# Performance work log

Hardware: AMD Instinct MI355X
Metric: run time of the kernel (lower is better)

Reference implementation:

```python
import jax, jax.numpy as jnp
import numpy as np

# SMPL kinematic tree parents (fixed, 24 joints)
PARENTS = (-1, 0, 0, 0, 1, 2, 3, 4, 5, 6, 7, 8, 9, 9, 9, 12, 13, 14, 16, 17, 18, 19, 20, 21)
RES = 64
B, N = 2, 32768


def _trilinear(grid, pts):
    """Faithful F.grid_sample (5D, bilinear, align_corners=False, zero padding).
    grid: [C, R, R, R]; pts: [M, 3] normalized coords in [-1, 1].
    After the permutes in correspondence_to_smpl_function, coordinate k of a
    point indexes spatial axis k of the stored grid. Returns [M, C]."""
    C, R = grid.shape[0], grid.shape[1]
    gt = grid.reshape(C, -1).T  # [R^3, C]
    coords = ((pts + 1.0) * R - 1.0) * 0.5  # align_corners=False unnormalize
    f0 = jnp.floor(coords)
    w1 = coords - f0
    w0 = 1.0 - w1
    i0 = f0.astype(jnp.int32)
    out = jnp.zeros((pts.shape[0], C), dtype=grid.dtype)
    for dx in (0, 1):
        for dy in (0, 1):
            for dz in (0, 1):
                ix, iy, iz = i0[:, 0] + dx, i0[:, 1] + dy, i0[:, 2] + dz
                valid = ((ix >= 0) & (ix < R) & (iy >= 0) & (iy < R)
                         & (iz >= 0) & (iz < R))
                w = ((w1[:, 0] if dx else w0[:, 0])
                     * (w1[:, 1] if dy else w0[:, 1])
                     * (w1[:, 2] if dz else w0[:, 2]))
                idx = (jnp.clip(ix, 0, R - 1) * R + jnp.clip(iy, 0, R - 1)) * R \
                      + jnp.clip(iz, 0, R - 1)
                out = out + gt[idx] * (w * valid.astype(w.dtype))[:, None]
    return out


def _rodrigues(r):
    """Axis-angle [J,3] -> rotation matrices [J,3,3] (matches th_posemap_axisang)."""
    theta = jnp.sqrt(jnp.sum(r * r, axis=-1) + 1e-12)  # [J]
    ax = r / theta[:, None]
    x, y, z = ax[:, 0], ax[:, 1], ax[:, 2]
    zero = jnp.zeros_like(x)
    K = jnp.stack([zero, -z, y, z, zero, -x, -y, x, zero], axis=-1).reshape(-1, 3, 3)
    s = jnp.sin(theta)[:, None, None]
    c = jnp.cos(theta)[:, None, None]
    I = jnp.eye(3, dtype=r.dtype)
    return I + s * K + (1.0 - c) * jnp.matmul(K, K)


def _skeleton(beta, rotmats, v_template, smpl_shapedirs, J_regressor):
    """compute_smpl_skeleton: returns relative joint transforms [B, 24, 4, 4]."""
    b = beta.shape[0]
    v = v_template[None] + jnp.einsum('vdk,bk->bvd', smpl_shapedirs, beta)  # [B,6890,3]
    j = jnp.einsum('jv,bvd->bjd', J_regressor, v)  # [B,24,3]
    bottom = jnp.tile(jnp.array([[[0., 0., 0., 1.]]], dtype=beta.dtype), (b, 1, 1))

    def mk(R, t):  # th_with_zeros
        return jnp.concatenate([jnp.concatenate([R, t[..., None]], -1), bottom], 1)

    results = [mk(rotmats[:, 0], j[:, 0])]
    for i in range(1, 24):  # fixed 24-joint chain
        p = PARENTS[i]
        rel = mk(rotmats[:, i], j[:, i] - j[:, p])
        results.append(jnp.matmul(results[p], rel))
    A = jnp.stack(results, axis=1)  # [B,24,4,4]
    # subtract th_pack(A @ [j;0]): only last column changes
    t = jnp.einsum('bjrc,bjc->bjr', A[..., :3], j)  # [B,24,4]
    return jnp.concatenate([A[..., :3], (A[..., 3] - t)[..., None]], -1)


def setup_inputs() -> dict:
    key = jax.random.key(0)
    ks = jax.random.split(key, 12)
    return {
        'points': jax.random.uniform(ks[0], (B, N, 3), jnp.float32, -0.9, 0.9),
        'pose': jax.random.normal(ks[1], (B, 72), jnp.float32) * 0.2,
        'beta': jax.random.normal(ks[2], (B, 10), jnp.float32),
        'trans': jax.random.normal(ks[3], (B, 3), jnp.float32) * 0.1,
        'scale': jnp.float32(1.0),
        'center': jnp.zeros((3,), jnp.float32),
        'closest_grid': jax.random.normal(ks[4], (3, RES, RES, RES), jnp.float32) * 0.5,
        'shapedirs_grid': jax.random.normal(ks[5], (30, RES, RES, RES), jnp.float32) * 0.01,
        'posedirs_grid': jax.random.normal(ks[6], (621, RES, RES, RES), jnp.float32) * 0.01,
        'skin_grid': jax.random.uniform(ks[7], (24, RES, RES, RES), jnp.float32),
        'v_template': jax.random.normal(ks[8], (6890, 3), jnp.float32) * 0.3,
        'smpl_shapedirs': jax.random.normal(ks[9], (6890, 3, 10), jnp.float32) * 0.01,
        'J_regressor': (lambda u: u / jnp.sum(u, 1, keepdims=True))(
            jax.random.uniform(ks[10], (24, 6890), jnp.float32)),
    }


def reference(points, pose, beta, trans, scale, center, closest_grid,
              shapedirs_grid, posedirs_grid, skin_grid, v_template,
              smpl_shapedirs, J_regressor):
    b, n = points.shape[0], points.shape[1]
    pts = (points * scale + center).reshape(-1, 3)  # [M,3]

    closest = _trilinear(closest_grid, pts).reshape(b, n, 3)
    shdirs = _trilinear(shapedirs_grid, pts).reshape(b, n, 3, 10)
    pdirs = _trilinear(posedirs_grid, pts).reshape(b, n, 3, 207)
    skin_w = _trilinear(skin_grid, pts).reshape(b, n, 24)

    rot = _rodrigues(pose.reshape(-1, 3)).reshape(b, 24, 3, 3)
    pose_map = (rot[:, 1:] - jnp.eye(3, dtype=rot.dtype)).reshape(b, 207)

    p_v_shaped = closest + jnp.einsum('bndk,bk->bnd', shdirs, beta)
    p_v_posed = p_v_shaped + jnp.einsum('bndk,bk->bnd', pdirs, pose_map)

    A = _skeleton(beta, rot, v_template, smpl_shapedirs, J_regressor)  # [B,24,4,4]
    A16 = jnp.transpose(A, (0, 2, 3, 1)).reshape(b, 16, 24)
    T = jnp.einsum('bkj,bnj->bnk', A16, skin_w).reshape(b, n, 4, 4)

    homog = jnp.concatenate([p_v_posed, jnp.ones((b, n, 1), p_v_posed.dtype)], -1)
    p_verts = jnp.einsum('bnrc,bnc->bnr', T, homog)[..., :3]
    return p_verts + trans[:, None, :]
```

## Files before the change

### kernel.cpp

```cpp
#include <hip/hip_runtime.h>


#define RES 64
#define VOX (RES * RES * RES)
#define BB 2
#define NN 32768
#define MM (BB * NN)

typedef unsigned short u16;
typedef unsigned int u32;

__device__ __forceinline__ float bfbits2f(u32 u) {
  union { u32 i; float f; } v; v.i = u << 16; return v.f;
}
__device__ __forceinline__ float bf2f(u16 u) { return bfbits2f((u32)u); }
__device__ __forceinline__ u16 f2bf(float f) {
  union { float f; u32 i; } v; v.f = f;
  u32 x = v.i;
  return (u16)((x + 0x7fffu + ((x >> 16) & 1u)) >> 16);
}
__device__ __forceinline__ void unpack8(const uint4 u, float* f) {
  f[0] = bfbits2f(u.x & 0xffffu); f[1] = bfbits2f(u.x >> 16);
  f[2] = bfbits2f(u.y & 0xffffu); f[3] = bfbits2f(u.y >> 16);
  f[4] = bfbits2f(u.z & 0xffffu); f[5] = bfbits2f(u.z >> 16);
  f[6] = bfbits2f(u.w & 0xffffu); f[7] = bfbits2f(u.w >> 16);
}

template <bool BF>
__device__ __forceinline__ float ld1(const void* p, size_t i) {
  if (BF) return bf2f(((const u16*)p)[i]);
  return ((const float*)p)[i];
}
template <bool BF>
__device__ __forceinline__ void ld8(const void* p, size_t i, float* f) {
  if (BF) {
    uint4 u = *(const uint4*)((const u16*)p + i);
    unpack8(u, f);
  } else {
    const float4* q = (const float4*)((const float*)p + i);
    float4 a = q[0], b = q[1];
    f[0] = a.x; f[1] = a.y; f[2] = a.z; f[3] = a.w;
    f[4] = b.x; f[5] = b.y; f[6] = b.z; f[7] = b.w;
  }
}

template <bool BF>
__device__ void joints_body(const void* beta, const void* vt, const void* sdirs,
                            const void* Jreg, float* jpos) {
  const int b = blockIdx.x / 24, jt = blockIdx.x % 24;
  float bet[10];
#pragma unroll
  for (int k = 0; k < 10; k++) bet[k] = ld1<BF>(beta, b * 10 + k);
  float s[3] = {0.f, 0.f, 0.f};
  for (int v = threadIdx.x; v < 6890; v += 256) {
    float jr = ld1<BF>(Jreg, (size_t)jt * 6890 + v);
#pragma unroll
    for (int dd = 0; dd < 3; dd++) {
      float val = ld1<BF>(vt, (size_t)v * 3 + dd);
      size_t sp = (size_t)(v * 3 + dd) * 10;
#pragma unroll
      for (int k = 0; k < 10; k++) val += ld1<BF>(sdirs, sp + k) * bet[k];
      s[dd] += jr * val;
    }
  }
#pragma unroll
  for (int off = 32; off >= 1; off >>= 1) {
    s[0] += __shfl_down(s[0], off);
    s[1] += __shfl_down(s[1], off);
    s[2] += __shfl_down(s[2], off);
  }
  __shared__ float red[4][3];
  int wave = threadIdx.x >> 6, lane = threadIdx.x & 63;
  if (lane == 0) { red[wave][0] = s[0]; red[wave][1] = s[1]; red[wave][2] = s[2]; }
  __syncthreads();
  if (threadIdx.x == 0) {
    for (int dd = 0; dd < 3; dd++)
      jpos[(b * 24 + jt) * 3 + dd] = red[0][dd] + red[1][dd] + red[2][dd] + red[3][dd];
  }
}
__global__ __launch_bounds__(256) void k_joints(
    const void* beta, const void* vt, const void* sdirs, const void* Jreg,
    float* jpos, const u16* probe) {
  if (probe[0]) joints_body<true>(beta, vt, sdirs, Jreg, jpos);
  else          joints_body<false>(beta, vt, sdirs, Jreg, jpos);
}

template <bool BF>
__device__ void pose_fk_body(const void* pose, const float* jpos,
                             float* pose_map, float* A12) {
  __shared__ float rot[BB * 24 * 9];
  __shared__ float AL[BB * 24 * 12];
  const int t = threadIdx.x;
  if (t < BB * 24) {
    int b = t / 24, jj = t % 24;
    float r0 = ld1<BF>(pose, b * 72 + jj * 3 + 0);
    float r1 = ld1<BF>(pose, b * 72 + jj * 3 + 1);
    float r2 = ld1<BF>(pose, b * 72 + jj * 3 + 2);
    float th = sqrtf(r0 * r0 + r1 * r1 + r2 * r2 + 1e-12f);
    float x = r0 / th, y = r1 / th, z = r2 / th;
    float sn = sinf(th), cs = cosf(th), cc = 1.0f - cs;
    float* R = &rot[t * 9];
    R[0] = 1.0f - cc * (y * y + z * z); R[1] = -sn * z + cc * x * y; R[2] =  sn * y + cc * x * z;
    R[3] =  sn * z + cc * x * y; R[4] = 1.0f - cc * (x * x + z * z); R[5] = -sn * x + cc * y * z;
    R[6] = -sn * y + cc * x * z; R[7] =  sn * x + cc * y * z; R[8] = 1.0f - cc * (x * x + y * y);
  }
  __syncthreads();
  for (int c = t; c < BB * 207; c += 64) {
    int b = c / 207, k = c % 207;
    int jj = k / 9 + 1, e = k % 9;
    pose_map[c] = rot[(b * 24 + jj) * 9 + e] - ((e == 0 || e == 4 || e == 8) ? 1.0f : 0.0f);
  }
  if (t < BB) {
    const int b = t;
    const int P[24] = {-1, 0, 0, 0, 1, 2, 3, 4, 5, 6, 7, 8, 9, 9, 9, 12, 13, 14, 16, 17, 18, 19, 20, 21};
    float R[24][9], Tt[24][3];
    for (int e = 0; e < 9; e++) R[0][e] = rot[(b * 24) * 9 + e];
    for (int dd = 0; dd < 3; dd++) Tt[0][dd] = jpos[(b * 24) * 3 + dd];
    for (int i = 1; i < 24; i++) {
      int p = P[i];
      float rl[9], tl[3];
      for (int e = 0; e < 9; e++) rl[e] = rot[(b * 24 + i) * 9 + e];
      for (int dd = 0; dd < 3; dd++) tl[dd] = jpos[(b * 24 + i) * 3 + dd] - jpos[(b * 24 + p) * 3 + dd];
      for (int r = 0; r < 3; r++) {
        for (int c2 = 0; c2 < 3; c2++) {
          R[i][r * 3 + c2] = R[p][r * 3 + 0] * rl[0 * 3 + c2] +
                             R[p][r * 3 + 1] * rl[1 * 3 + c2] +
                             R[p][r * 3 + 2] * rl[2 * 3 + c2];
        }
        Tt[i][r] = Tt[p][r] + R[p][r * 3 + 0] * tl[0] + R[p][r * 3 + 1] * tl[1] + R[p][r * 3 + 2] * tl[2];
      }
    }
    for (int i = 0; i < 24; i++) {
      float jx = jpos[(b * 24 + i) * 3 + 0];
      float jy = jpos[(b * 24 + i) * 3 + 1];
      float jz = jpos[(b * 24 + i) * 3 + 2];
      for (int r = 0; r < 3; r++) {
        float trv = Tt[i][r] - (R[i][r * 3 + 0] * jx + R[i][r * 3 + 1] * jy + R[i][r * 3 + 2] * jz);
        float* o = &AL[(b * 24 + i) * 12 + r * 4];
        o[0] = R[i][r * 3 + 0]; o[1] = R[i][r * 3 + 1]; o[2] = R[i][r * 3 + 2]; o[3] = trv;
      }
    }
  }
  __syncthreads();
  for (int c = t; c < BB * 12 * 24; c += 64) {
    int b = c / 288, rest = c % 288, rc = rest / 24, jj = rest % 24;
    A12[c] = AL[(b * 24 + jj) * 12 + rc];
  }
}
__global__ __launch_bounds__(64) void k_pose_fk(
    const void* pose, const float* jpos, float* pose_map, float* A12,
    const u16* probe) {
  if (probe[0]) pose_fk_body<true>(pose, jpos, pose_map, A12);
  else          pose_fk_body<false>(pose, jpos, pose_map, A12);
}

template <bool BF>
__device__ void skinT_body(const void* skin, void* skinT) {
  const int idx = blockIdx.x * 256 + threadIdx.x;
  if (BF) {
    const u16* s = (const u16*)skin;
    u32 pk[12];
#pragma unroll
    for (int c = 0; c < 12; c++) {
      u32 lo = s[(size_t)(2 * c) * VOX + idx];
      u32 hi = s[(size_t)(2 * c + 1) * VOX + idx];
      pk[c] = lo | (hi << 16);
    }
    uint4* dst = (uint4*)((u16*)skinT + (size_t)idx * 24);
    dst[0] = make_uint4(pk[0], pk[1], pk[2], pk[3]);
    dst[1] = make_uint4(pk[4], pk[5], pk[6], pk[7]);
    dst[2] = make_uint4(pk[8], pk[9], pk[10], pk[11]);
  } else {
    const float* s = (const float*)skin;
    float* dst = (float*)skinT + (size_t)idx * 24;
#pragma unroll
    for (int c = 0; c < 24; c++) dst[c] = s[(size_t)c * VOX + idx];
  }
}
__global__ __launch_bounds__(256) void k_skinT(const void* skin, void* skinT,
                                               const u16* probe) {
  if (probe[0]) skinT_body<true>(skin, skinT);
  else          skinT_body<false>(skin, skinT);
}

template <bool BF>
__device__ void gpos_body(const void* closest, const void* shdirs,
                          const void* pdirs, const void* beta,
                          const float* __restrict__ pose_map,
                          float* __restrict__ Gpos) {
  __shared__ float pm[BB * 207];
  __shared__ float bet[BB * 10];
  const int t = threadIdx.x;
  const int d = blockIdx.y;
  for (int c = t; c < BB * 207; c += 128) pm[c] = pose_map[c];
  if (t < BB * 10) bet[t] = ld1<BF>(beta, t);
  __syncthreads();
  const int idx0 = blockIdx.x * 1024 + t * 8;
  float a0[8], a1[8], f[8];
  ld8<BF>(closest, (size_t)d * VOX + idx0, f);
#pragma unroll
  for (int v = 0; v < 8; v++) { a0[v] = f[v]; a1[v] = f[v]; }
#pragma unroll
  for (int k = 0; k < 10; k++) {
    ld8<BF>(shdirs, (size_t)(d * 10 + k) * VOX + idx0, f);
    float b0 = bet[k], b1 = bet[10 + k];
#pragma unroll
    for (int v = 0; v < 8; v++) { a0[v] += f[v] * b0; a1[v] += f[v] * b1; }
  }
  const size_t pbase = (size_t)(d * 207) * VOX + idx0;
#pragma unroll 3
  for (int k = 0; k < 207; k++) {
    ld8<BF>(pdirs, pbase + (size_t)k * VOX, f);
    float p0 = pm[k], p1 = pm[207 + k];
#pragma unroll
    for (int v = 0; v < 8; v++) { a0[v] += f[v] * p0; a1[v] += f[v] * p1; }
  }
  float* o0 = Gpos + (size_t)(0 * 3 + d) * VOX + idx0;
  float* o1 = Gpos + (size_t)(1 * 3 + d) * VOX + idx0;
  *(float4*)(o0)     = make_float4(a0[0], a0[1], a0[2], a0[3]);
  *(float4*)(o0 + 4) = make_float4(a0[4], a0[5], a0[6], a0[7]);
  *(float4*)(o1)     = make_float4(a1[0], a1[1], a1[2], a1[3]);
  *(float4*)(o1 + 4) = make_float4(a1[4], a1[5], a1[6], a1[7]);
}
__global__ __launch_bounds__(128) void k_gpos(
    const void* closest, const void* shdirs, const void* pdirs,
    const void* beta, const float* pose_map, float* Gpos, const u16* probe) {
  if (probe[0]) gpos_body<true>(closest, shdirs, pdirs, beta, pose_map, Gpos);
  else          gpos_body<false>(closest, shdirs, pdirs, beta, pose_map, Gpos);
}

template <bool BF, bool FULLP>
__device__ void points_body(const void* points, const void* scale,
                            const void* center, const void* trans,
                            const float* __restrict__ Gpos, const void* skinT,
                            const void* skin, const float* __restrict__ A12,
                            void* out) {
  __shared__ float A[BB * 12 * 24];
  __shared__ float tr[BB * 3];
  const int t = threadIdx.x;
  for (int c = t; c < BB * 12 * 24; c += 256) A[c] = A12[c];
  if (t < BB * 3) tr[t] = ld1<BF>(trans, t);
  __syncthreads();
  const int m = blockIdx.x * 256 + t;
  const int b = m >> 15;
  const float sc = ld1<BF>(scale, 0);
  float w0[3], w1[3];
  int i0[3];
#pragma unroll
  for (int dd = 0; dd < 3; dd++) {
    float p = ld1<BF>(points, (size_t)m * 3 + dd) * sc + ld1<BF>(center, dd);
    float c = ((p + 1.0f) * (float)RES - 1.0f) * 0.5f;
    float f0 = floorf(c);
    w1[dd] = c - f0;
    w0[dd] = 1.0f - w1[dd];
    i0[dd] = (int)f0;
  }
  float pos[3] = {0.f, 0.f, 0.f};
  float sw[24];
#pragma unroll
  for (int j = 0; j < 24; j++) sw[j] = 0.f;
#pragma unroll
  for (int corner = 0; corner < 8; corner++) {
    int dx = (corner >> 2) & 1, dy = (corner >> 1) & 1, dz = corner & 1;
    int ix = i0[0] + dx, iy = i0[1] + dy, iz = i0[2] + dz;
    bool valid = (ix >= 0) && (ix < RES) && (iy >= 0) && (iy < RES) &&
                 (iz >= 0) && (iz < RES);
    float w = (dx ? w1[0] : w0[0]) * (dy ? w1[1] : w0[1]) * (dz ? w1[2] : w0[2]);
    w = valid ? w : 0.0f;
    int cx = min(max(ix, 0), RES - 1);
    int cy = min(max(iy, 0), RES - 1);
    int cz = min(max(iz, 0), RES - 1);
    int idx = (cx * RES + cy) * RES + cz;
    pos[0] += w * Gpos[(size_t)(b * 3 + 0) * VOX + idx];
    pos[1] += w * Gpos[(size_t)(b * 3 + 1) * VOX + idx];
    pos[2] += w * Gpos[(size_t)(b * 3 + 2) * VOX + idx];
    float f[24];
    if (FULLP) {
      if (BF) {
        const uint4* sp = (const uint4*)((const u16*)skinT + (size_t)idx * 24);
        uint4 u0 = sp[0], u1 = sp[1], u2 = sp[2];
        unpack8(u0, f); unpack8(u1, f + 8); unpack8(u2, f + 16);
      } else {
        const float4* sp = (const float4*)((const float*)skinT + (size_t)idx * 24);
#pragma unroll
        for (int q = 0; q < 6; q++) {
          float4 v = sp[q];
          f[q * 4 + 0] = v.x; f[q * 4 + 1] = v.y; f[q * 4 + 2] = v.z; f[q * 4 + 3] = v.w;
        }
      }
    } else {
#pragma unroll
      for (int j = 0; j < 24; j++) f[j] = ld1<BF>(skin, (size_t)j * VOX + idx);
    }
#pragma unroll
    for (int j = 0; j < 24; j++) sw[j] += w * f[j];
  }
  const float* Ab = A + b * 288;
  float T[12];
#pragma unroll
  for (int rc = 0; rc < 12; rc++) {
    float a = 0.f;
    const float* Ar = Ab + rc * 24;
#pragma unroll
    for (int j = 0; j < 24; j++) a += Ar[j] * sw[j];
    T[rc] = a;
  }
#pragma unroll
  for (int r = 0; r < 3; r++) {
    float o = T[r * 4 + 0] * pos[0] + T[r * 4 + 1] * pos[1] +
              T[r * 4 + 2] * pos[2] + T[r * 4 + 3] + tr[b * 3 + r];
    if (BF) ((u16*)out)[(size_t)m * 3 + r] = f2bf(o);
    else    ((float*)out)[(size_t)m * 3 + r] = o;
  }
}
__global__ __launch_bounds__(256) void k_points_full(
    const void* points, const void* scale, const void* center, const void* trans,
    const float* Gpos, const void* skinT, const void* skin, const float* A12,
    void* out, const u16* probe) {
  if (probe[0]) points_body<true, true>(points, scale, center, trans, Gpos, skinT, skin, A12, out);
  else          points_body<false, true>(points, scale, center, trans, Gpos, skinT, skin, A12, out);
}
__global__ __launch_bounds__(256) void k_points_mid(
    const void* points, const void* scale, const void* center, const void* trans,
    const float* Gpos, const void* skinT, const void* skin, const float* A12,
    void* out, const u16* probe) {
  if (probe[0]) points_body<true, false>(points, scale, center, trans, Gpos, skinT, skin, A12, out);
  else          points_body<false, false>(points, scale, center, trans, Gpos, skinT, skin, A12, out);
}

extern "C" void kernel_launch(void* const* d_in, const int* in_sizes, int n_in,
                              void* d_out, int out_size, void* d_ws, size_t ws_size,
                              hipStream_t stream) {
  const void* points  = d_in[0];
  const void* pose    = d_in[1];
  const void* beta    = d_in[2];
  const void* trans   = d_in[3];
  const void* scale   = d_in[4];
  const void* center  = d_in[5];
  const void* closest = d_in[6];
  const void* shdirs  = d_in[7];
  const void* pdirs   = d_in[8];
  const void* skin    = d_in[9];
  const void* vt      = d_in[10];
  const void* sdirs   = d_in[11];
  const void* Jreg    = d_in[12];
  const u16* probe = (const u16*)scale;

  const size_t GPOS_B  = (size_t)BB * 3 * VOX * 4;
  const size_t SKINT_B = (size_t)VOX * 24 * 4;
  const size_t SMALL_B = 1656 + 576 + 2304;
  const bool full = ws_size >= GPOS_B + SKINT_B + SMALL_B;

  char* ws = (char*)d_ws;
  float* Gpos = (float*)ws;
  void* skinT = ws + GPOS_B;
  char* small = ws + (full ? GPOS_B + SKINT_B : GPOS_B);
  float* pose_map = (float*)small;
  float* jpos     = (float*)(small + 1656);
  float* A12      = (float*)(small + 1656 + 576);

  hipLaunchKernelGGL(k_joints, dim3(48), dim3(256), 0, stream,
                     beta, vt, sdirs, Jreg, jpos, probe);
  hipLaunchKernelGGL(k_pose_fk, dim3(1), dim3(64), 0, stream,
                     pose, jpos, pose_map, A12, probe);
  if (full) {
    hipLaunchKernelGGL(k_skinT, dim3(VOX / 256), dim3(256), 0, stream,
                       skin, skinT, probe);
  }
  hipLaunchKernelGGL(k_gpos, dim3(VOX / 1024, 3), dim3(128), 0, stream,
                     closest, shdirs, pdirs, beta, pose_map, Gpos, probe);
  if (full) {
    hipLaunchKernelGGL(k_points_full, dim3(MM / 256), dim3(256), 0, stream,
                       points, scale, center, trans, Gpos, skinT, skin, A12,
                       d_out, probe);
  } else {
    hipLaunchKernelGGL(k_points_mid, dim3(MM / 256), dim3(256), 0, stream,
                       points, scale, center, trans, Gpos, skinT, skin, A12,
                       d_out, probe);
  }
}
```

Baseline: 1.042 ms.

## Precompute per-voxel skinning transform grid and widen gpos block parallelism

Replaces the skin-weight transpose with a kernel that multiplies the 24 skin weights by the joint transforms per voxel, producing a 12-float transform grid per batch. The points kernel then interpolates those 12 values instead of 24 weights and skips the per-point 12x24 matrix product. This relies on linearity of trilinear interpolation. Separately, the gpos kernel now has each thread handle 4 voxels with 256 threads per block instead of 8 voxels with 128, giving more threads in flight over the large pdirs stream. The transform grid needs more workspace (2x12 floats per voxel) and costs extra write traffic over all voxels.

```diff
diff --git a/kernel.cpp b/kernel.cpp
--- a/kernel.cpp
+++ b/kernel.cpp
@@ -32,15 +32,14 @@
   return ((const float*)p)[i];
 }
 template <bool BF>
-__device__ __forceinline__ void ld8(const void* p, size_t i, float* f) {
+__device__ __forceinline__ void ld4v(const void* p, size_t i, float* f) {
   if (BF) {
-    uint4 u = *(const uint4*)((const u16*)p + i);
-    unpack8(u, f);
+    uint2 u = *(const uint2*)((const u16*)p + i);
+    f[0] = bfbits2f(u.x & 0xffffu); f[1] = bfbits2f(u.x >> 16);
+    f[2] = bfbits2f(u.y & 0xffffu); f[3] = bfbits2f(u.y >> 16);
   } else {
-    const float4* q = (const float4*)((const float*)p + i);
-    float4 a = q[0], b = q[1];
+    float4 a = *(const float4*)((const float*)p + i);
     f[0] = a.x; f[1] = a.y; f[2] = a.z; f[3] = a.w;
-    f[4] = b.x; f[5] = b.y; f[6] = b.z; f[7] = b.w;
   }
 }
 
@@ -155,32 +154,38 @@
 }
 
 template <bool BF>
-__device__ void skinT_body(const void* skin, void* skinT) {
-  const int idx = blockIdx.x * 256 + threadIdx.x;
-  if (BF) {
-    const u16* s = (const u16*)skin;
-    u32 pk[12];
-#pragma unroll
-    for (int c = 0; c < 12; c++) {
-      u32 lo = s[(size_t)(2 * c) * VOX + idx];
-      u32 hi = s[(size_t)(2 * c + 1) * VOX + idx];
-      pk[c] = lo | (hi << 16);
+__device__ void tgrid_body(const void* skin, const float* __restrict__ A12,
+                           float* __restrict__ Tg) {
+  __shared__ float A[BB * 12 * 24];
+  for (int c = threadIdx.x; c < BB * 12 * 24; c += 256) A[c] = A12[c];
+  __syncthreads();
+  const int vox = blockIdx.x * 256 + threadIdx.x;
+  float acc0[12], acc1[12];
+#pragma unroll
+  for (int rc = 0; rc < 12; rc++) { acc0[rc] = 0.f; acc1[rc] = 0.f; }
+#pragma unroll 4
+  for (int j = 0; j < 24; j++) {
+    float s = ld1<BF>(skin, (size_t)j * VOX + vox);
+#pragma unroll
+    for (int rc = 0; rc < 12; rc++) {
+      acc0[rc] += A[rc * 24 + j] * s;
+      acc1[rc] += A[288 + rc * 24 + j] * s;
     }
-    uint4* dst = (uint4*)((u16*)skinT + (size_t)idx * 24);
-    dst[0] = make_uint4(pk[0], pk[1], pk[2], pk[3]);
-    dst[1] = make_uint4(pk[4], pk[5], pk[6], pk[7]);
-    dst[2] = make_uint4(pk[8], pk[9], pk[10], pk[11]);
-  } else {
-    const float* s = (const float*)skin;
-    float* dst = (float*)skinT + (size_t)idx * 24;
-#pragma unroll
-    for (int c = 0; c < 24; c++) dst[c] = s[(size_t)c * VOX + idx];
-  }
-}
-__global__ __launch_bounds__(256) void k_skinT(const void* skin, void* skinT,
+  }
+  float4* o0 = (float4*)(Tg + (size_t)vox * 12);
+  float4* o1 = (float4*)(Tg + ((size_t)VOX + vox) * 12);
+  o0[0] = make_float4(acc0[0], acc0[1], acc0[2], acc0[3]);
+  o0[1] = make_float4(acc0[4], acc0[5], acc0[6], acc0[7]);
+  o0[2] = make_float4(acc0[8], acc0[9], acc0[10], acc0[11]);
+  o1[0] = make_float4(acc1[0], acc1[1], acc1[2], acc1[3]);
+  o1[1] = make_float4(acc1[4], acc1[5], acc1[6], acc1[7]);
+  o1[2] = make_float4(acc1[8], acc1[9], acc1[10], acc1[11]);
+}
+__global__ __launch_bounds__(256) void k_tgrid(const void* skin,
+                                               const float* A12, float* Tg,
                                                const u16* probe) {
-  if (probe[0]) skinT_body<true>(skin, skinT);
-  else          skinT_body<false>(skin, skinT);
+  if (probe[0]) tgrid_body<true>(skin, A12, Tg);
+  else          tgrid_body<false>(skin, A12, Tg);
 }
 
 template <bool BF>
@@ -192,49 +197,113 @@
   __shared__ float bet[BB * 10];
   const int t = threadIdx.x;
   const int d = blockIdx.y;
-  for (int c = t; c < BB * 207; c += 128) pm[c] = pose_map[c];
+  for (int c = t; c < BB * 207; c += 256) pm[c] = pose_map[c];
   if (t < BB * 10) bet[t] = ld1<BF>(beta, t);
   __syncthreads();
-  const int idx0 = blockIdx.x * 1024 + t * 8;
-  float a0[8], a1[8], f[8];
-  ld8<BF>(closest, (size_t)d * VOX + idx0, f);
-#pragma unroll
-  for (int v = 0; v < 8; v++) { a0[v] = f[v]; a1[v] = f[v]; }
+  const int idx0 = blockIdx.x * 1024 + t * 4;
+  float a0[4], a1[4], f[4];
+  ld4v<BF>(closest, (size_t)d * VOX + idx0, f);
+#pragma unroll
+  for (int v = 0; v < 4; v++) { a0[v] = f[v]; a1[v] = f[v]; }
 #pragma unroll
   for (int k = 0; k < 10; k++) {
-    ld8<BF>(shdirs, (size_t)(d * 10 + k) * VOX + idx0, f);
+    ld4v<BF>(shdirs, (size_t)(d * 10 + k) * VOX + idx0, f);
     float b0 = bet[k], b1 = bet[10 + k];
 #pragma unroll
-    for (int v = 0; v < 8; v++) { a0[v] += f[v] * b0; a1[v] += f[v] * b1; }
+    for (int v = 0; v < 4; v++) { a0[v] += f[v] * b0; a1[v] += f[v] * b1; }
   }
   const size_t pbase = (size_t)(d * 207) * VOX + idx0;
 #pragma unroll 3
   for (int k = 0; k < 207; k++) {
-    ld8<BF>(pdirs, pbase + (size_t)k * VOX, f);
+    ld4v<BF>(pdirs, pbase + (size_t)k * VOX, f);
     float p0 = pm[k], p1 = pm[207 + k];
 #pragma unroll
-    for (int v = 0; v < 8; v++) { a0[v] += f[v] * p0; a1[v] += f[v] * p1; }
+    for (int v = 0; v < 4; v++) { a0[v] += f[v] * p0; a1[v] += f[v] * p1; }
   }
   float* o0 = Gpos + (size_t)(0 * 3 + d) * VOX + idx0;
   float* o1 = Gpos + (size_t)(1 * 3 + d) * VOX + idx0;
-  *(float4*)(o0)     = make_float4(a0[0], a0[1], a0[2], a0[3]);
-  *(float4*)(o0 + 4) = make_float4(a0[4], a0[5], a0[6], a0[7]);
-  *(float4*)(o1)     = make_float4(a1[0], a1[1], a1[2], a1[3]);
-  *(float4*)(o1 + 4) = make_float4(a1[4], a1[5], a1[6], a1[7]);
-}
-__global__ __launch_bounds__(128) void k_gpos(
+  *(float4*)(o0) = make_float4(a0[0], a0[1], a0[2], a0[3]);
+  *(float4*)(o1) = make_float4(a1[0], a1[1], a1[2], a1[3]);
+}
+__global__ __launch_bounds__(256) void k_gpos(
     const void* closest, const void* shdirs, const void* pdirs,
     const void* beta, const float* pose_map, float* Gpos, const u16* probe) {
   if (probe[0]) gpos_body<true>(closest, shdirs, pdirs, beta, pose_map, Gpos);
   else          gpos_body<false>(closest, shdirs, pdirs, beta, pose_map, Gpos);
 }
 
-template <bool BF, bool FULLP>
-__device__ void points_body(const void* points, const void* scale,
-                            const void* center, const void* trans,
-                            const float* __restrict__ Gpos, const void* skinT,
-                            const void* skin, const float* __restrict__ A12,
-                            void* out) {
+template <bool BF>
+__device__ void points_full_body(const void* points, const void* scale,
+                                 const void* center, const void* trans,
+                                 const float* __restrict__ Gpos,
+                                 const float* __restrict__ Tg, void* out) {
+  const int t = threadIdx.x;
+  __shared__ float tr[BB * 3];
+  if (t < BB * 3) tr[t] = ld1<BF>(trans, t);
+  __syncthreads();
+  const int m = blockIdx.x * 256 + t;
+  const int b = m >> 15;
+  const float sc = ld1<BF>(scale, 0);
+  float w0[3], w1[3];
+  int i0[3];
+#pragma unroll
+  for (int dd = 0; dd < 3; dd++) {
+    float p = ld1<BF>(points, (size_t)m * 3 + dd) * sc + ld1<BF>(center, dd);
+    float c = ((p + 1.0f) * (float)RES - 1.0f) * 0.5f;
+    float f0 = floorf(c);
+    w1[dd] = c - f0;
+    w0[dd] = 1.0f - w1[dd];
+    i0[dd] = (int)f0;
+  }
+  const float* G0 = Gpos + (size_t)(b * 3 + 0) * VOX;
+  const float* G1 = G0 + VOX;
+  const float* G2 = G1 + VOX;
+  const float* Tb = Tg + (size_t)b * VOX * 12;
+  float pos[3] = {0.f, 0.f, 0.f};
+  float T[12];
+#pragma unroll
+  for (int rc = 0; rc < 12; rc++) T[rc] = 0.f;
+#pragma unroll
+  for (int corner = 0; corner < 8; corner++) {
+    int dx = (corner >> 2) & 1, dy = (corner >> 1) & 1, dz = corner & 1;
+    int ix = i0[0] + dx, iy = i0[1] + dy, iz = i0[2] + dz;
+    bool valid = (ix >= 0) && (ix < RES) && (iy >= 0) && (iy < RES) &&
+                 (iz >= 0) && (iz < RES);
+    float w = (dx ? w1[0] : w0[0]) * (dy ? w1[1] : w0[1]) * (dz ? w1[2] : w0[2]);
+    w = valid ? w : 0.0f;
+    int cx = min(max(ix, 0), RES - 1);
+    int cy = min(max(iy, 0), RES - 1);
+    int cz = min(max(iz, 0), RES - 1);
+    int idx = (cx * RES + cy) * RES + cz;
+    pos[0] += w * G0[idx];
+    pos[1] += w * G1[idx];
+    pos[2] += w * G2[idx];
+    const float4* tp = (const float4*)(Tb + (size_t)idx * 12);
+    float4 q0 = tp[0], q1 = tp[1], q2 = tp[2];
+    T[0] += w * q0.x; T[1] += w * q0.y; T[2]  += w * q0.z; T[3]  += w * q0.w;
+    T[4] += w * q1.x; T[5] += w * q1.y; T[6]  += w * q1.z; T[7]  += w * q1.w;
+    T[8] += w * q2.x; T[9] += w * q2.y; T[10] += w * q2.z; T[11] += w * q2.w;
+  }
+#pragma unroll
+  for (int r = 0; r < 3; r++) {
+    float o = T[r * 4 + 0] * pos[0] + T[r * 4 + 1] * pos[1] +
+              T[r * 4 + 2] * pos[2] + T[r * 4 + 3] + tr[b * 3 + r];
+    if (BF) ((u16*)out)[(size_t)m * 3 + r] = f2bf(o);
+    else    ((float*)out)[(size_t)m * 3 + r] = o;
+  }
+}
+__global__ __launch_bounds__(256) void k_points_full(
+    const void* points, const void* scale, const void* center, const void* trans,
+    const float* Gpos, const float* Tg, void* out, const u16* probe) {
+  if (probe[0]) points_full_body<true>(points, scale, center, trans, Gpos, Tg, out);
+  else          points_full_body<false>(points, scale, center, trans, Gpos, Tg, out);
+}
+
+template <bool BF>
+__device__ void points_mid_body(const void* points, const void* scale,
+                                const void* center, const void* trans,
+                                const float* __restrict__ Gpos, const void* skin,
+                                const float* __restrict__ A12, void* out) {
   __shared__ float A[BB * 12 * 24];
   __shared__ float tr[BB * 3];
   const int t = threadIdx.x;
@@ -274,26 +343,8 @@
     pos[0] += w * Gpos[(size_t)(b * 3 + 0) * VOX + idx];
     pos[1] += w * Gpos[(size_t)(b * 3 + 1) * VOX + idx];
     pos[2] += w * Gpos[(size_t)(b * 3 + 2) * VOX + idx];
-    float f[24];
-    if (FULLP) {
-      if (BF) {
-        const uint4* sp = (const uint4*)((const u16*)skinT + (size_t)idx * 24);
-        uint4 u0 = sp[0], u1 = sp[1], u2 = sp[2];
-        unpack8(u0, f); unpack8(u1, f + 8); unpack8(u2, f + 16);
-      } else {
-        const float4* sp = (const float4*)((const float*)skinT + (size_t)idx * 24);
-#pragma unroll
-        for (int q = 0; q < 6; q++) {
-          float4 v = sp[q];
-          f[q * 4 + 0] = v.x; f[q * 4 + 1] = v.y; f[q * 4 + 2] = v.z; f[q * 4 + 3] = v.w;
-        }
-      }
-    } else {
-#pragma unroll
-      for (int j = 0; j < 24; j++) f[j] = ld1<BF>(skin, (size_t)j * VOX + idx);
-    }
-#pragma unroll
-    for (int j = 0; j < 24; j++) sw[j] += w * f[j];
+#pragma unroll
+    for (int j = 0; j < 24; j++) sw[j] += w * ld1<BF>(skin, (size_t)j * VOX + idx);
   }
   const float* Ab = A + b * 288;
   float T[12];
@@ -313,19 +364,12 @@
     else    ((float*)out)[(size_t)m * 3 + r] = o;
   }
 }
-__global__ __launch_bounds__(256) void k_points_full(
-    const void* points, const void* scale, const void* center, const void* trans,
-    const float* Gpos, const void* skinT, const void* skin, const float* A12,
-    void* out, const u16* probe) {
-  if (probe[0]) points_body<true, true>(points, scale, center, trans, Gpos, skinT, skin, A12, out);
-  else          points_body<false, true>(points, scale, center, trans, Gpos, skinT, skin, A12, out);
-}
 __global__ __launch_bounds__(256) void k_points_mid(
     const void* points, const void* scale, const void* center, const void* trans,
-    const float* Gpos, const void* skinT, const void* skin, const float* A12,
-    void* out, const u16* probe) {
-  if (probe[0]) points_body<true, false>(points, scale, center, trans, Gpos, skinT, skin, A12, out);
-  else          points_body<false, false>(points, scale, center, trans, Gpos, skinT, skin, A12, out);
+    const float* Gpos, const void* skin, const float* A12, void* out,
+    const u16* probe) {
+  if (probe[0]) points_mid_body<true>(points, scale, center, trans, Gpos, skin, A12, out);
+  else          points_mid_body<false>(points, scale, center, trans, Gpos, skin, A12, out);
 }
 
 extern "C" void kernel_launch(void* const* d_in, const int* in_sizes, int n_in,
@@ -346,15 +390,15 @@
   const void* Jreg    = d_in[12];
   const u16* probe = (const u16*)scale;
 
-  const size_t GPOS_B  = (size_t)BB * 3 * VOX * 4;
-  const size_t SKINT_B = (size_t)VOX * 24 * 4;
+  const size_t GPOS_B = (size_t)BB * 3 * VOX * 4;
+  const size_t TG_B   = (size_t)BB * VOX * 12 * 4;
   const size_t SMALL_B = 1656 + 576 + 2304;
-  const bool full = ws_size >= GPOS_B + SKINT_B + SMALL_B;
+  const bool full = ws_size >= GPOS_B + TG_B + SMALL_B;
 
   char* ws = (char*)d_ws;
   float* Gpos = (float*)ws;
-  void* skinT = ws + GPOS_B;
-  char* small = ws + (full ? GPOS_B + SKINT_B : GPOS_B);
+  float* Tg   = (float*)(ws + GPOS_B);
+  char* small = ws + (full ? GPOS_B + TG_B : GPOS_B);
   float* pose_map = (float*)small;
   float* jpos     = (float*)(small + 1656);
   float* A12      = (float*)(small + 1656 + 576);
@@ -364,18 +408,17 @@
   hipLaunchKernelGGL(k_pose_fk, dim3(1), dim3(64), 0, stream,
                      pose, jpos, pose_map, A12, probe);
   if (full) {
-    hipLaunchKernelGGL(k_skinT, dim3(VOX / 256), dim3(256), 0, stream,
-                       skin, skinT, probe);
-  }
-  hipLaunchKernelGGL(k_gpos, dim3(VOX / 1024, 3), dim3(128), 0, stream,
+    hipLaunchKernelGGL(k_tgrid, dim3(VOX / 256), dim3(256), 0, stream,
+                       skin, A12, Tg, probe);
+  }
+  hipLaunchKernelGGL(k_gpos, dim3(VOX / 1024, 3), dim3(256), 0, stream,
                      closest, shdirs, pdirs, beta, pose_map, Gpos, probe);
   if (full) {
     hipLaunchKernelGGL(k_points_full, dim3(MM / 256), dim3(256), 0, stream,
-                       points, scale, center, trans, Gpos, skinT, skin, A12,
-                       d_out, probe);
+                       points, scale, center, trans, Gpos, Tg, d_out, probe);
   } else {
     hipLaunchKernelGGL(k_points_mid, dim3(MM / 256), dim3(256), 0, stream,
-                       points, scale, center, trans, Gpos, skinT, skin, A12,
-                       d_out, probe);
-  }
-}
+                       points, scale, center, trans, Gpos, skin, A12, d_out,
+                       probe);
+  }
+}
```

After: 960.0 us. 7.9% less time.
